# Kernel tuning notes

Measured on AMD Instinct MI355X. Metric: run time of the kernel, lower is better.

Reference implementation:

```python
import jax, jax.numpy as jnp
import numpy as np

K_NEIGHBORS = 16
NUM_PATCHES = 32
W_NORMAL = 1.0
W_SURFVAR = 1.0


def _knn_centered(points, k):
    """points: [B, N, 3] -> k nearest neighbors re-centered at each point, [B, N, k, 3].
    Distances are computed on stop_gradient(points) to match torch's .detach()."""
    pd = jax.lax.stop_gradient(points)
    # squared pairwise distances [B, N, N] (sqrt is monotone -> topk order identical)
    d2 = jnp.sum((pd[:, :, None, :] - pd[:, None, :, :]) ** 2, axis=-1)
    _, idx = jax.lax.top_k(-d2, k)  # smallest-k indices, [B, N, k]
    knn = jax.vmap(lambda pts, id_: pts[id_])(points, idx)  # [B, N, k, 3]
    return knn - points[:, :, None, :]


def _eig_props(knn):
    """knn: [B, N, k, 3] -> (normal [B,N,3] = eigvec of smallest eigval, eigvals [B,N,3] ascending)."""
    cov = jnp.einsum('bnki,bnkj->bnij', knn, knn)  # [B, N, 3, 3]
    w, v = jnp.linalg.eigh(cov)  # ascending eigenvalues, matches torch.symeig
    return v[..., :, 0], w


def setup_inputs() -> dict:
    key = jax.random.key(0)
    pointCloud = jax.random.normal(key, (4, 8192, 3), dtype=jnp.float32)
    return {"pointCloud": pointCloud}


def reference(pointCloud):
    B, N, _ = pointCloud.shape
    pp = N // NUM_PATCHES

    # global kNN / normals / surface variance
    knn_g = _knn_centered(pointCloud, K_NEIGHBORS)
    nrm_g, w_g = _eig_props(knn_g)

    # patchwise: each patch is an independent small point cloud -> fold patches into batch
    patch_pts = pointCloud.reshape(B * NUM_PATCHES, pp, 3)
    knn_p = _knn_centered(patch_pts, K_NEIGHBORS)
    nrm_p, w_p = _eig_props(knn_p)
    nrm_p = nrm_p.reshape(B, N, 3)

    # normal loss (abs variant, sign-ambiguity-free)
    loss_n = jnp.mean(jnp.linalg.norm(jnp.abs(nrm_p) - jnp.abs(nrm_g), axis=2)) * W_NORMAL

    # surface variance loss: lambda_min / sum(lambda)
    sv_g = w_g[..., 0] / jnp.sum(w_g, axis=-1)            # [B, N]
    sv_p = (w_p[..., 0] / jnp.sum(w_p, axis=-1)).reshape(B, N)
    loss_sv = jnp.mean((sv_p - sv_g) ** 2) * W_SURFVAR

    return jnp.stack([loss_n, loss_sv])  # [2] (original returns list of two [1] tensors)
```

## Files before the change

### kernel.cpp

```cpp
#include <hip/hip_runtime.h>
#include <math.h>

#define KNN 16
#define NPTS 8192
#define PTCH 256
#define NPATCH 32
#define NBATCH 4
#define NQ 32
#define TILE 1024
#define SSTRIDE 130
#define LAMBDA_T 64.0f

__global__ void zero2_kernel(float* out) { out[0] = 0.0f; out[1] = 0.0f; }

__device__ __forceinline__ float lam_f(float r, float s)
{
    const float C     = 0.063493636f;
    const float SQ2PI = 2.5066283f;
    const float IS2   = 0.70710678f;
    float a = fabsf(r - s), b = r + s;
    float amr = a - r;
    float coefA = amr * amr + 2.f - s * s;
    float I = 2.f * __expf(-0.5f * b * b) - coefA * __expf(-0.5f * a * a)
            + r * SQ2PI * (erff(b * IS2) - erff(a * IS2));
    float M = C * (3.14159265f / r) * I;
    if (s > r) {
        float u = s - r;
        M += 12.566371f * C * (1.2533141f * erff(u * IS2) - u * __expf(-0.5f * u * u));
    }
    return (float)NPTS * M;
}

__device__ __forceinline__ void jrot(double& app, double& aqq, double& apq,
                                     double& arp, double& arq,
                                     double& vp0, double& vq0,
                                     double& vp1, double& vq1,
                                     double& vp2, double& vq2)
{
    double g = apq;
    if (g == 0.0) return;
    double theta = (aqq - app) / (2.0 * g);
    double at = fabs(theta);
    double t = (at > 1.0e154) ? (0.5 / theta)
                              : (copysign(1.0, theta) / (at + sqrt(theta * theta + 1.0)));
    double c = 1.0 / sqrt(t * t + 1.0);
    double s = t * c;
    double tau = s / (1.0 + c);
    app -= t * g;
    aqq += t * g;
    apq = 0.0;
    double rp = arp, rq = arq;
    arp = rp - s * (rq + tau * rp);
    arq = rq + s * (rp - tau * rq);
    double p0 = vp0, q0 = vq0;
    vp0 = p0 - s * (q0 + tau * p0); vq0 = q0 + s * (p0 - tau * q0);
    double p1 = vp1, q1 = vq1;
    vp1 = p1 - s * (q1 + tau * p1); vq1 = q1 + s * (p1 - tau * q1);
    double p2 = vp2, q2 = vq2;
    vp2 = p2 - s * (q2 + tau * p2); vq2 = q2 + s * (p2 - tau * q2);
}

__device__ __forceinline__ void eig3(double a00, double a11, double a22,
                                     double a01, double a02, double a12,
                                     double& nx, double& ny, double& nz,
                                     double& lmin, double& lsum)
{
    double v00 = 1, v01 = 0, v02 = 0;
    double v10 = 0, v11 = 1, v12 = 0;
    double v20 = 0, v21 = 0, v22 = 1;
    double scale = fabs(a00) + fabs(a11) + fabs(a22) + fabs(a01) + fabs(a02) + fabs(a12);
    if (scale > 0.0) {
        for (int sweep = 0; sweep < 6; ++sweep) {
            double off = fabs(a01) + fabs(a02) + fabs(a12);
            if (off <= scale * 1e-15) break;
            jrot(a00, a11, a01, a02, a12, v00, v01, v10, v11, v20, v21);
            jrot(a00, a22, a02, a01, a12, v00, v02, v10, v12, v20, v22);
            jrot(a11, a22, a12, a01, a02, v01, v02, v11, v12, v21, v22);
        }
    }
    lsum = a00 + a11 + a22;
    lmin = a00; nx = v00; ny = v10; nz = v20;
    if (a11 < lmin) { lmin = a11; nx = v01; ny = v11; nz = v21; }
    if (a22 < lmin) { lmin = a22; nx = v02; ny = v12; nz = v22; }
}

__device__ __forceinline__ unsigned mkkey(float d2, unsigned idx) {
    return (__float_as_uint(d2) & 0xFFFFE000u) | idx;
}

__device__ __forceinline__ void insert16(unsigned key, unsigned* L)
{
    L[KNN - 1] = key;
    #pragma unroll
    for (int m = KNN - 1; m >= 1; --m) {
        unsigned a = L[m - 1], b = L[m];
        L[m - 1] = min(a, b);
        L[m]     = max(a, b);
    }
}

__device__ __forceinline__ void merge4(unsigned* L, int lane)
{
    #pragma unroll
    for (int step = 1; step <= 2; step <<= 1) {
        unsigned tmp[KNN];
        #pragma unroll
        for (int m = 0; m < KNN; ++m) tmp[m] = __shfl(L[m], lane ^ step, 64);
        for (int m = 0; m < KNN; ++m) {
            if (tmp[m] >= L[KNN - 1]) break;
            insert16(tmp[m], L);
        }
    }
}

__device__ __forceinline__ float rfl(float x) {
    return __int_as_float(__builtin_amdgcn_readfirstlane(__float_as_int(x)));
}
__device__ __forceinline__ unsigned mbcnt64(unsigned long long m) {
    return __builtin_amdgcn_mbcnt_hi((unsigned)(m >> 32),
           __builtin_amdgcn_mbcnt_lo((unsigned)m, 0u));
}

__global__ void __launch_bounds__(256, 4)
spl_main(const float* __restrict__ pts, float* __restrict__ out)
{
    __shared__ float4 tile4[TILE];
    __shared__ float4 pbuf4[PTCH];
    __shared__ unsigned short surv[NQ * SSTRIDE];
    __shared__ unsigned cnts[NQ];
    __shared__ float gbuf[NQ];
    __shared__ double xbuf[NQ * 4];
    __shared__ double rb[4];

    const int t = threadIdx.x;
    const int w = t >> 6;
    const int lane = t & 63;
    const int p = blockIdx.x;
    const int eighth = blockIdx.y;
    const int b = blockIdx.z;

    const float* base = pts + (size_t)b * (NPTS * 3);
    const int qbase = p * PTCH + eighth * NQ;

    {
        const float* src = base + p * (PTCH * 3);
        float* dst = (float*)pbuf4;
        #pragma unroll
        for (int s = 0; s < 3; ++s) {
            int f = t + s * 256;
            int j = f / 3;
            int c = f - 3 * j;
            dst[j * 4 + c] = src[f];
        }
    }
    if (t < NQ) {
        int qi = qbase + t;
        float x = base[qi * 3 + 0], y = base[qi * 3 + 1], z = base[qi * 3 + 2];
        float r = fmaxf(sqrtf(x * x + y * y + z * z), 0.01f);
        float lo = 0.f, hi = 12.f;
        #pragma unroll 1
        for (int it = 0; it < 16; ++it) {
            float mid = 0.5f * (lo + hi);
            if (lam_f(r, mid) < LAMBDA_T) lo = mid; else hi = mid;
        }
        gbuf[t] = hi * hi;
    }
    __syncthreads();

    float sqx[8], sqy[8], sqz[8], shq[8];
    unsigned scnt[8];
    #pragma unroll
    for (int u = 0; u < 8; ++u) {
        float4 qv = pbuf4[eighth * NQ + w * 8 + u];
        float gg = gbuf[w * 8 + u];
        sqx[u] = rfl(qv.x); sqy[u] = rfl(qv.y); sqz[u] = rfl(qv.z);
        shq[u] = rfl(0.5f * (gg - (qv.x * qv.x + qv.y * qv.y + qv.z * qv.z)));
        scnt[u] = 0;
    }

    #pragma unroll 1
    for (int tb = 0; tb < NPTS; tb += TILE) {
        __syncthreads();
        {
            const float* src = base + tb * 3;
            float* dst = (float*)tile4;
            #pragma unroll
            for (int s = 0; s < 12; ++s) {
                int f = t + s * 256;
                int j = f / 3;
                int c = f - 3 * j;
                dst[j * 4 + c] = src[f];
            }
        }
        __syncthreads();
        float4 c = tile4[lane];
        #pragma unroll 1
        for (int it = 0; it < TILE / 64; ++it) {
            float4 cn = tile4[min(it + 1, TILE / 64 - 1) * 64 + lane];
            float hn = 0.5f * (c.x * c.x + c.y * c.y + c.z * c.z);
            unsigned gidx = (unsigned)(tb + it * 64 + lane);
            #pragma unroll
            for (int u = 0; u < 8; ++u) {
                float tt = fmaf(-c.x, sqx[u], hn);
                tt = fmaf(-c.y, sqy[u], tt);
                tt = fmaf(-c.z, sqz[u], tt);
                bool pass = tt < shq[u];
                unsigned long long m = __ballot(pass);
                if (m) {
                    unsigned pre = mbcnt64(m);
                    if (pass) {
                        unsigned slot = min(scnt[u] + pre, (unsigned)(SSTRIDE - 1));
                        surv[(w * 8 + u) * SSTRIDE + slot] = (unsigned short)gidx;
                    }
                    scnt[u] += (unsigned)__popcll(m);
                }
            }
            c = cn;
        }
    }
    if (lane == 0) {
        #pragma unroll
        for (int u = 0; u < 8; ++u) cnts[w * 8 + u] = scnt[u];
    }
    __syncthreads();

    const int qq = lane >> 2;
    const int h = lane & 3;
    const int myq = (w & 1) * 16 + qq;
    float4 qv = pbuf4[eighth * NQ + myq];
    const float pqx = qv.x, pqy = qv.y, pqz = qv.z;

    double ngx = 0, ngy = 0, ngz = 0, svg = 0;

    if (w < 2) {
        unsigned gl[KNN];
        #pragma unroll
        for (int m = 0; m < KNN; ++m) gl[m] = 0xFFFFFFFFu;
        unsigned cnt = cnts[myq];
        bool valid = (cnt >= KNN) && (cnt <= SSTRIDE);
        if (valid) {
            unsigned share = (cnt + 3) >> 2;
            unsigned m0 = h * share;
            unsigned m1 = min(m0 + share, cnt);
            #pragma unroll 1
            for (unsigned m = m0; m < m1; ++m) {
                unsigned idx = surv[myq * SSTRIDE + m];
                float cx = base[idx * 3 + 0];
                float cy = base[idx * 3 + 1];
                float cz = base[idx * 3 + 2];
                float dx = pqx - cx, dy = pqy - cy, dz = pqz - cz;
                float d2 = dx * dx + dy * dy + dz * dz;
                unsigned k = mkkey(d2, idx);
                if (k < gl[KNN - 1]) insert16(k, gl);
            }
        }
        merge4(gl, lane);
        if (valid) {
            float g = gbuf[myq];
            float upper = __uint_as_float((gl[KNN - 1] & 0xFFFFE000u) + 0x2000u);
            valid = (upper < g * 0.999f - 1e-5f);
        }
        if (__any((h == 0 && !valid) ? 1 : 0)) {
            if (h == 0 && !valid) {
                #pragma unroll
                for (int m = 0; m < KNN; ++m) gl[m] = 0xFFFFFFFFu;
                #pragma unroll 1
                for (int i = 0; i < NPTS; ++i) {
                    float cx = base[i * 3 + 0];
                    float cy = base[i * 3 + 1];
                    float cz = base[i * 3 + 2];
                    float dx = pqx - cx, dy = pqy - cy, dz = pqz - cz;
                    float d2 = dx * dx + dy * dy + dz * dz;
                    unsigned k = mkkey(d2, (unsigned)i);
                    if (k < gl[KNN - 1]) insert16(k, gl);
                }
            }
        }
        if (h == 0) {
            double c00 = 0, c11 = 0, c22 = 0, c01 = 0, c02 = 0, c12 = 0;
            const double qxd = pqx, qyd = pqy, qzd = pqz;
            #pragma unroll
            for (int m = 0; m < KNN; ++m) {
                int idx = (int)(gl[m] & 0x1FFFu);
                double dx = (double)base[idx * 3 + 0] - qxd;
                double dy = (double)base[idx * 3 + 1] - qyd;
                double dz = (double)base[idx * 3 + 2] - qzd;
                c00 += dx * dx; c11 += dy * dy; c22 += dz * dz;
                c01 += dx * dy; c02 += dx * dz; c12 += dy * dz;
            }
            double lmin, lsum;
            eig3(c00, c11, c22, c01, c02, c12, ngx, ngy, ngz, lmin, lsum);
            svg = lmin / lsum;
        }
    } else {
        unsigned pl[KNN];
        #pragma unroll
        for (int m = 0; m < KNN; ++m) pl[m] = 0xFFFFFFFFu;
        const int j0 = h * 64;
        #pragma unroll 1
        for (int j = j0; j < j0 + 64; ++j) {
            float4 c = pbuf4[j];
            float dx = pqx - c.x, dy = pqy - c.y, dz = pqz - c.z;
            float d2 = dx * dx + dy * dy + dz * dz;
            unsigned k = mkkey(d2, (unsigned)j);
            if (k < pl[KNN - 1]) insert16(k, pl);
        }
        merge4(pl, lane);
        if (h == 0) {
            double c00 = 0, c11 = 0, c22 = 0, c01 = 0, c02 = 0, c12 = 0;
            const double qxd = pqx, qyd = pqy, qzd = pqz;
            #pragma unroll
            for (int m = 0; m < KNN; ++m) {
                int idx = (int)(pl[m] & 0x1FFFu);
                float4 cpt = pbuf4[idx];
                double dx = (double)cpt.x - qxd;
                double dy = (double)cpt.y - qyd;
                double dz = (double)cpt.z - qzd;
                c00 += dx * dx; c11 += dy * dy; c22 += dz * dz;
                c01 += dx * dy; c02 += dx * dz; c12 += dy * dz;
            }
            double nx, ny, nz, lmin, lsum;
            eig3(c00, c11, c22, c01, c02, c12, nx, ny, nz, lmin, lsum);
            xbuf[myq * 4 + 0] = nx;
            xbuf[myq * 4 + 1] = ny;
            xbuf[myq * 4 + 2] = nz;
            xbuf[myq * 4 + 3] = lmin / lsum;
        }
    }
    __syncthreads();

    double ln = 0.0, lsv = 0.0;
    if (w < 2 && h == 0) {
        double npx = xbuf[myq * 4 + 0];
        double npy = xbuf[myq * 4 + 1];
        double npz = xbuf[myq * 4 + 2];
        double svp = xbuf[myq * 4 + 3];
        double dx = fabs(npx) - fabs(ngx);
        double dy = fabs(npy) - fabs(ngy);
        double dz = fabs(npz) - fabs(ngz);
        ln  = sqrt(dx * dx + dy * dy + dz * dz);
        double ds = svp - svg;
        lsv = ds * ds;
    }
    if (w < 2) {
        #pragma unroll
        for (int o = 32; o > 0; o >>= 1) {
            ln  += __shfl_down(ln, o);
            lsv += __shfl_down(lsv, o);
        }
        if (lane == 0) { rb[w * 2 + 0] = ln; rb[w * 2 + 1] = lsv; }
    }
    __syncthreads();
    if (t == 0) {
        const double inv = 1.0 / (double)(NBATCH * NPTS);
        atomicAdd(&out[0], (float)((rb[0] + rb[2]) * inv));
        atomicAdd(&out[1], (float)((rb[1] + rb[3]) * inv));
    }
}

extern "C" void kernel_launch(void* const* d_in, const int* in_sizes, int n_in,
                              void* d_out, int out_size, void* d_ws, size_t ws_size,
                              hipStream_t stream)
{
    const float* pts = (const float*)d_in[0];
    float* out = (float*)d_out;
    hipLaunchKernelGGL(zero2_kernel, dim3(1), dim3(1), 0, stream, out);
    dim3 grid(NPATCH, 8, NBATCH);
    hipLaunchKernelGGL(spl_main, grid, dim3(256), 0, stream, pts, out);
}
```

Baseline: 162.2 us.

## Halve queries per block, double grid, switch eigen solve to float

Each block now handles 16 queries instead of 32, which doubles the grid and spreads neighbor search across 8 lanes per query with an 8-way shuffle merge. The Jacobi eigen-solver and covariance accumulation move from double to float, and the launch-bounds occupancy hint goes from 4 to 6. The zeroing kernel is replaced by hipMemsetAsync. The aim is more parallelism and fewer slow FP64 operations, at the cost of reloading each point tile in twice as many blocks and lower precision in the normals and surface variance.

```diff
diff --git a/kernel.cpp b/kernel.cpp
--- a/kernel.cpp
+++ b/kernel.cpp
@@ -6,12 +6,10 @@
 #define PTCH 256
 #define NPATCH 32
 #define NBATCH 4
-#define NQ 32
+#define NQ 16
 #define TILE 1024
 #define SSTRIDE 130
 #define LAMBDA_T 64.0f
-
-__global__ void zero2_kernel(float* out) { out[0] = 0.0f; out[1] = 0.0f; }
 
 __device__ __forceinline__ float lam_f(float r, float s)
 {
@@ -31,51 +29,51 @@
     return (float)NPTS * M;
 }
 
-__device__ __forceinline__ void jrot(double& app, double& aqq, double& apq,
-                                     double& arp, double& arq,
-                                     double& vp0, double& vq0,
-                                     double& vp1, double& vq1,
-                                     double& vp2, double& vq2)
-{
-    double g = apq;
-    if (g == 0.0) return;
-    double theta = (aqq - app) / (2.0 * g);
-    double at = fabs(theta);
-    double t = (at > 1.0e154) ? (0.5 / theta)
-                              : (copysign(1.0, theta) / (at + sqrt(theta * theta + 1.0)));
-    double c = 1.0 / sqrt(t * t + 1.0);
-    double s = t * c;
-    double tau = s / (1.0 + c);
+__device__ __forceinline__ void jrotf(float& app, float& aqq, float& apq,
+                                      float& arp, float& arq,
+                                      float& vp0, float& vq0,
+                                      float& vp1, float& vq1,
+                                      float& vp2, float& vq2)
+{
+    float g = apq;
+    if (g == 0.f) return;
+    float theta = (aqq - app) / (2.f * g);
+    float at = fabsf(theta);
+    float t = (at > 1.0e18f) ? (0.5f / theta)
+                             : (copysignf(1.f, theta) / (at + sqrtf(theta * theta + 1.f)));
+    float c = 1.f / sqrtf(t * t + 1.f);
+    float s = t * c;
+    float tau = s / (1.f + c);
     app -= t * g;
     aqq += t * g;
-    apq = 0.0;
-    double rp = arp, rq = arq;
+    apq = 0.f;
+    float rp = arp, rq = arq;
     arp = rp - s * (rq + tau * rp);
     arq = rq + s * (rp - tau * rq);
-    double p0 = vp0, q0 = vq0;
+    float p0 = vp0, q0 = vq0;
     vp0 = p0 - s * (q0 + tau * p0); vq0 = q0 + s * (p0 - tau * q0);
-    double p1 = vp1, q1 = vq1;
+    float p1 = vp1, q1 = vq1;
     vp1 = p1 - s * (q1 + tau * p1); vq1 = q1 + s * (p1 - tau * q1);
-    double p2 = vp2, q2 = vq2;
+    float p2 = vp2, q2 = vq2;
     vp2 = p2 - s * (q2 + tau * p2); vq2 = q2 + s * (p2 - tau * q2);
 }
 
-__device__ __forceinline__ void eig3(double a00, double a11, double a22,
-                                     double a01, double a02, double a12,
-                                     double& nx, double& ny, double& nz,
-                                     double& lmin, double& lsum)
-{
-    double v00 = 1, v01 = 0, v02 = 0;
-    double v10 = 0, v11 = 1, v12 = 0;
-    double v20 = 0, v21 = 0, v22 = 1;
-    double scale = fabs(a00) + fabs(a11) + fabs(a22) + fabs(a01) + fabs(a02) + fabs(a12);
-    if (scale > 0.0) {
+__device__ __forceinline__ void eig3f(float a00, float a11, float a22,
+                                      float a01, float a02, float a12,
+                                      float& nx, float& ny, float& nz,
+                                      float& lmin, float& lsum)
+{
+    float v00 = 1, v01 = 0, v02 = 0;
+    float v10 = 0, v11 = 1, v12 = 0;
+    float v20 = 0, v21 = 0, v22 = 1;
+    float scale = fabsf(a00) + fabsf(a11) + fabsf(a22) + fabsf(a01) + fabsf(a02) + fabsf(a12);
+    if (scale > 0.f) {
         for (int sweep = 0; sweep < 6; ++sweep) {
-            double off = fabs(a01) + fabs(a02) + fabs(a12);
-            if (off <= scale * 1e-15) break;
-            jrot(a00, a11, a01, a02, a12, v00, v01, v10, v11, v20, v21);
-            jrot(a00, a22, a02, a01, a12, v00, v02, v10, v12, v20, v22);
-            jrot(a11, a22, a12, a01, a02, v01, v02, v11, v12, v21, v22);
+            float off = fabsf(a01) + fabsf(a02) + fabsf(a12);
+            if (off <= scale * 1e-7f) break;
+            jrotf(a00, a11, a01, a02, a12, v00, v01, v10, v11, v20, v21);
+            jrotf(a00, a22, a02, a01, a12, v00, v02, v10, v12, v20, v22);
+            jrotf(a11, a22, a12, a01, a02, v01, v02, v11, v12, v21, v22);
         }
     }
     lsum = a00 + a11 + a22;
@@ -99,10 +97,10 @@
     }
 }
 
-__device__ __forceinline__ void merge4(unsigned* L, int lane)
+__device__ __forceinline__ void merge8(unsigned* L, int lane)
 {
     #pragma unroll
-    for (int step = 1; step <= 2; step <<= 1) {
+    for (int step = 1; step <= 4; step <<= 1) {
         unsigned tmp[KNN];
         #pragma unroll
         for (int m = 0; m < KNN; ++m) tmp[m] = __shfl(L[m], lane ^ step, 64);
@@ -121,7 +119,7 @@
            __builtin_amdgcn_mbcnt_lo((unsigned)m, 0u));
 }
 
-__global__ void __launch_bounds__(256, 4)
+__global__ void __launch_bounds__(256, 6)
 spl_main(const float* __restrict__ pts, float* __restrict__ out)
 {
     __shared__ float4 tile4[TILE];
@@ -129,18 +127,17 @@
     __shared__ unsigned short surv[NQ * SSTRIDE];
     __shared__ unsigned cnts[NQ];
     __shared__ float gbuf[NQ];
-    __shared__ double xbuf[NQ * 4];
+    __shared__ float xbuf[NQ * 4];
     __shared__ double rb[4];
 
     const int t = threadIdx.x;
     const int w = t >> 6;
     const int lane = t & 63;
     const int p = blockIdx.x;
-    const int eighth = blockIdx.y;
+    const int six = blockIdx.y;
     const int b = blockIdx.z;
 
     const float* base = pts + (size_t)b * (NPTS * 3);
-    const int qbase = p * PTCH + eighth * NQ;
 
     {
         const float* src = base + p * (PTCH * 3);
@@ -154,7 +151,7 @@
         }
     }
     if (t < NQ) {
-        int qi = qbase + t;
+        int qi = p * PTCH + six * NQ + t;
         float x = base[qi * 3 + 0], y = base[qi * 3 + 1], z = base[qi * 3 + 2];
         float r = fmaxf(sqrtf(x * x + y * y + z * z), 0.01f);
         float lo = 0.f, hi = 12.f;
@@ -167,12 +164,12 @@
     }
     __syncthreads();
 
-    float sqx[8], sqy[8], sqz[8], shq[8];
-    unsigned scnt[8];
+    float sqx[4], sqy[4], sqz[4], shq[4];
+    unsigned scnt[4];
     #pragma unroll
-    for (int u = 0; u < 8; ++u) {
-        float4 qv = pbuf4[eighth * NQ + w * 8 + u];
-        float gg = gbuf[w * 8 + u];
+    for (int u = 0; u < 4; ++u) {
+        float4 qv = pbuf4[six * NQ + w * 4 + u];
+        float gg = gbuf[w * 4 + u];
         sqx[u] = rfl(qv.x); sqy[u] = rfl(qv.y); sqz[u] = rfl(qv.z);
         shq[u] = rfl(0.5f * (gg - (qv.x * qv.x + qv.y * qv.y + qv.z * qv.z)));
         scnt[u] = 0;
@@ -200,7 +197,7 @@
             float hn = 0.5f * (c.x * c.x + c.y * c.y + c.z * c.z);
             unsigned gidx = (unsigned)(tb + it * 64 + lane);
             #pragma unroll
-            for (int u = 0; u < 8; ++u) {
+            for (int u = 0; u < 4; ++u) {
                 float tt = fmaf(-c.x, sqx[u], hn);
                 tt = fmaf(-c.y, sqy[u], tt);
                 tt = fmaf(-c.z, sqz[u], tt);
@@ -210,7 +207,7 @@
                     unsigned pre = mbcnt64(m);
                     if (pass) {
                         unsigned slot = min(scnt[u] + pre, (unsigned)(SSTRIDE - 1));
-                        surv[(w * 8 + u) * SSTRIDE + slot] = (unsigned short)gidx;
+                        surv[(w * 4 + u) * SSTRIDE + slot] = (unsigned short)gidx;
                     }
                     scnt[u] += (unsigned)__popcll(m);
                 }
@@ -220,17 +217,17 @@
     }
     if (lane == 0) {
         #pragma unroll
-        for (int u = 0; u < 8; ++u) cnts[w * 8 + u] = scnt[u];
+        for (int u = 0; u < 4; ++u) cnts[w * 4 + u] = scnt[u];
     }
     __syncthreads();
 
-    const int qq = lane >> 2;
-    const int h = lane & 3;
-    const int myq = (w & 1) * 16 + qq;
-    float4 qv = pbuf4[eighth * NQ + myq];
+    const int qq = lane >> 3;
+    const int h = lane & 7;
+    const int myq = (w & 1) * 8 + qq;
+    float4 qv = pbuf4[six * NQ + myq];
     const float pqx = qv.x, pqy = qv.y, pqz = qv.z;
 
-    double ngx = 0, ngy = 0, ngz = 0, svg = 0;
+    float ngx = 0.f, ngy = 0.f, ngz = 0.f, svg = 0.f;
 
     if (w < 2) {
         unsigned gl[KNN];
@@ -239,7 +236,7 @@
         unsigned cnt = cnts[myq];
         bool valid = (cnt >= KNN) && (cnt <= SSTRIDE);
         if (valid) {
-            unsigned share = (cnt + 3) >> 2;
+            unsigned share = (cnt + 7) >> 3;
             unsigned m0 = h * share;
             unsigned m1 = min(m0 + share, cnt);
             #pragma unroll 1
@@ -254,7 +251,7 @@
                 if (k < gl[KNN - 1]) insert16(k, gl);
             }
         }
-        merge4(gl, lane);
+        merge8(gl, lane);
         if (valid) {
             float g = gbuf[myq];
             float upper = __uint_as_float((gl[KNN - 1] & 0xFFFFE000u) + 0x2000u);
@@ -277,50 +274,48 @@
             }
         }
         if (h == 0) {
-            double c00 = 0, c11 = 0, c22 = 0, c01 = 0, c02 = 0, c12 = 0;
-            const double qxd = pqx, qyd = pqy, qzd = pqz;
+            float c00 = 0, c11 = 0, c22 = 0, c01 = 0, c02 = 0, c12 = 0;
             #pragma unroll
             for (int m = 0; m < KNN; ++m) {
                 int idx = (int)(gl[m] & 0x1FFFu);
-                double dx = (double)base[idx * 3 + 0] - qxd;
-                double dy = (double)base[idx * 3 + 1] - qyd;
-                double dz = (double)base[idx * 3 + 2] - qzd;
+                float dx = base[idx * 3 + 0] - pqx;
+                float dy = base[idx * 3 + 1] - pqy;
+                float dz = base[idx * 3 + 2] - pqz;
                 c00 += dx * dx; c11 += dy * dy; c22 += dz * dz;
                 c01 += dx * dy; c02 += dx * dz; c12 += dy * dz;
             }
-            double lmin, lsum;
-            eig3(c00, c11, c22, c01, c02, c12, ngx, ngy, ngz, lmin, lsum);
+            float lmin, lsum;
+            eig3f(c00, c11, c22, c01, c02, c12, ngx, ngy, ngz, lmin, lsum);
             svg = lmin / lsum;
         }
     } else {
         unsigned pl[KNN];
         #pragma unroll
         for (int m = 0; m < KNN; ++m) pl[m] = 0xFFFFFFFFu;
-        const int j0 = h * 64;
+        const int j0 = h * 32;
         #pragma unroll 1
-        for (int j = j0; j < j0 + 64; ++j) {
+        for (int j = j0; j < j0 + 32; ++j) {
             float4 c = pbuf4[j];
             float dx = pqx - c.x, dy = pqy - c.y, dz = pqz - c.z;
             float d2 = dx * dx + dy * dy + dz * dz;
             unsigned k = mkkey(d2, (unsigned)j);
             if (k < pl[KNN - 1]) insert16(k, pl);
         }
-        merge4(pl, lane);
+        merge8(pl, lane);
         if (h == 0) {
-            double c00 = 0, c11 = 0, c22 = 0, c01 = 0, c02 = 0, c12 = 0;
-            const double qxd = pqx, qyd = pqy, qzd = pqz;
+            float c00 = 0, c11 = 0, c22 = 0, c01 = 0, c02 = 0, c12 = 0;
             #pragma unroll
             for (int m = 0; m < KNN; ++m) {
                 int idx = (int)(pl[m] & 0x1FFFu);
                 float4 cpt = pbuf4[idx];
-                double dx = (double)cpt.x - qxd;
-                double dy = (double)cpt.y - qyd;
-                double dz = (double)cpt.z - qzd;
+                float dx = cpt.x - pqx;
+                float dy = cpt.y - pqy;
+                float dz = cpt.z - pqz;
                 c00 += dx * dx; c11 += dy * dy; c22 += dz * dz;
                 c01 += dx * dy; c02 += dx * dz; c12 += dy * dz;
             }
-            double nx, ny, nz, lmin, lsum;
-            eig3(c00, c11, c22, c01, c02, c12, nx, ny, nz, lmin, lsum);
+            float nx, ny, nz, lmin, lsum;
+            eig3f(c00, c11, c22, c01, c02, c12, nx, ny, nz, lmin, lsum);
             xbuf[myq * 4 + 0] = nx;
             xbuf[myq * 4 + 1] = ny;
             xbuf[myq * 4 + 2] = nz;
@@ -330,19 +325,19 @@
     __syncthreads();
 
     double ln = 0.0, lsv = 0.0;
-    if (w < 2 && h == 0) {
-        double npx = xbuf[myq * 4 + 0];
-        double npy = xbuf[myq * 4 + 1];
-        double npz = xbuf[myq * 4 + 2];
-        double svp = xbuf[myq * 4 + 3];
-        double dx = fabs(npx) - fabs(ngx);
-        double dy = fabs(npy) - fabs(ngy);
-        double dz = fabs(npz) - fabs(ngz);
-        ln  = sqrt(dx * dx + dy * dy + dz * dz);
-        double ds = svp - svg;
-        lsv = ds * ds;
-    }
     if (w < 2) {
+        if (h == 0) {
+            double npx = xbuf[myq * 4 + 0];
+            double npy = xbuf[myq * 4 + 1];
+            double npz = xbuf[myq * 4 + 2];
+            double svp = xbuf[myq * 4 + 3];
+            double dx = fabs(npx) - fabs((double)ngx);
+            double dy = fabs(npy) - fabs((double)ngy);
+            double dz = fabs(npz) - fabs((double)ngz);
+            ln  = sqrt(dx * dx + dy * dy + dz * dz);
+            double ds = svp - (double)svg;
+            lsv = ds * ds;
+        }
         #pragma unroll
         for (int o = 32; o > 0; o >>= 1) {
             ln  += __shfl_down(ln, o);
@@ -364,7 +359,7 @@
 {
     const float* pts = (const float*)d_in[0];
     float* out = (float*)d_out;
-    hipLaunchKernelGGL(zero2_kernel, dim3(1), dim3(1), 0, stream, out);
-    dim3 grid(NPATCH, 8, NBATCH);
+    hipMemsetAsync(out, 0, 2 * sizeof(float), stream);
+    dim3 grid(NPATCH, 16, NBATCH);
     hipLaunchKernelGGL(spl_main, grid, dim3(256), 0, stream, pts, out);
 }
```

Result: slower. 182.0 us (+12.2%).
